# Performance work log

Measured on AMD Instinct MI355X. Metric: run time of the kernel, lower is better.

Reference implementation:

```python
import jax, jax.numpy as jnp
import numpy as np

NF = 16   # channels (nf)
HID = 32  # radial MLP hidden
L = 3     # n_layers
EPS = 1e-8


def fully_connected(N):
    # matches connect_fully(): all (i,j), i != j, row-major over src i
    idx = np.arange(N)
    src, dst = np.meshgrid(idx, idx, indexing='ij')
    mask = src != dst
    return jnp.asarray(src[mask]), jnp.asarray(dst[mask])


def setup_inputs() -> dict:
    key = jax.random.key(0)
    ks = jax.random.split(key, 12)
    B, N, c = 32, 64, NF
    return {
        "pos": jax.random.normal(ks[0], (B * N, 3), jnp.float32),
        "v": jax.random.normal(ks[1], (B * N, 3), jnp.float32),
        "z": jax.random.uniform(ks[2], (B * N,), jnp.float32),
        "w_s_in": jax.random.normal(ks[3], (1, c), jnp.float32) * 0.5,
        "w_v_in": jax.random.normal(ks[4], (1, c), jnp.float32) * 0.5,
        "radial_w1": jax.random.normal(ks[5], (L, 1, HID), jnp.float32) * 0.5,
        "radial_b1": jnp.zeros((L, HID), jnp.float32),
        "radial_w2": jax.random.normal(ks[6], (L, HID, 4 * c * c), jnp.float32) * (1.0 / np.sqrt(HID)),
        "radial_b2": jnp.zeros((L, 4 * c * c), jnp.float32),
        "self_ws": jax.random.normal(ks[7], (L, c, c), jnp.float32) * (1.0 / np.sqrt(c)),
        "self_wv": jax.random.normal(ks[8], (L, c, c), jnp.float32) * (1.0 / np.sqrt(c)),
        "w_v_out": jax.random.normal(ks[9], (c, 1), jnp.float32) * (1.0 / np.sqrt(c)),
        "B": 32,
        "N": 64,
    }


def _tfn_forward(pos, v, z, w_s_in, w_v_in, radial_w1, radial_b1,
                 radial_w2, radial_b2, self_ws, self_wv, w_v_out, B, N):
    c = NF
    src, dst = fully_connected(N)              # [E], E = N*(N-1)
    xs = pos.reshape(B, N, 3)
    vs = v.reshape(B, N, 3)
    # degree-0 (scalar) and degree-1 (vector) node features
    s = z.reshape(B, N, 1) @ w_s_in                                  # [B,N,c]
    vec = vs[:, :, None, :] * w_v_in[0][None, None, :, None]        # [B,N,c,3]
    # per-edge relative geometry (xs[dst] - xs[src], as in source)
    d = xs[:, dst] - xs[:, src]                                      # [B,E,3]
    r = jnp.linalg.norm(d, axis=-1, keepdims=True)                   # [B,E,1]
    u = d / (r + EPS)                                                # unit dir
    for l in range(L):
        # radial network -> per-edge kernel weights (TFN radial kernels)
        h = jax.nn.relu(r @ radial_w1[l] + radial_b1[l])             # [B,E,HID]
        k = h @ radial_w2[l] + radial_b2[l]                          # [B,E,4*c*c]
        W = k.reshape(B, k.shape[1], 4, c, c)
        Wss, Wsv, Wvs, Wvv = W[:, :, 0], W[:, :, 1], W[:, :, 2], W[:, :, 3]
        s_src = s[:, src]                                            # [B,E,c]
        v_src = vec[:, src]                                          # [B,E,c,3]
        v_dot = jnp.einsum('becd,bed->bec', v_src, u)                # 1->0 contraction
        # messages (equivariant): scalar and vector channels
        m_s = jnp.einsum('beij,bej->bei', Wss, s_src) \
            + jnp.einsum('beij,bej->bei', Wvs, v_dot)                # [B,E,c]
        m_v = jnp.einsum('beij,bejd->beid', Wvv, v_src) \
            + jnp.einsum('beij,bej->bei', Wsv, s_src)[..., None] * u[:, :, None, :]  # [B,E,c,3]
        # scatter-aggregate onto destination nodes
        agg_s = jnp.zeros_like(s).at[:, dst].add(m_s)
        agg_v = jnp.zeros_like(vec).at[:, dst].add(m_v)
        # self-interaction + residual (ReLU only on invariant channels)
        s = jax.nn.relu(agg_s @ self_ws[l]) + s
        vec = jnp.einsum('bncd,ce->bned', agg_v, self_wv[l]) + vec
    out_v = jnp.einsum('bncd,c->bnd', vec, w_v_out[:, 0])            # [B,N,3]  (G_out['1'])
    return (out_v + xs).reshape(-1, 3)                               # data.x


def reference(pos, v, z, w_s_in, w_v_in, radial_w1, radial_b1,
              radial_w2, radial_b2, self_ws, self_wv, w_v_out, B, N):
    return _tfn_forward(pos, v, z, w_s_in, w_v_in, radial_w1, radial_b1,
                        radial_w2, radial_b2, self_ws, self_wv, w_v_out, B, N)
```

## Files before the change

kernel.cpp:

```cpp
#include <hip/hip_runtime.h>

#define NF 16
#define NB 32
#define NN 64
#define EPSV 1e-8f

typedef _Float16 f16x8 __attribute__((ext_vector_type(8)));
typedef _Float16 f16x2 __attribute__((ext_vector_type(2)));
typedef __fp16 fp16x2 __attribute__((ext_vector_type(2)));
typedef float f32x4 __attribute__((ext_vector_type(4)));

#define SA_OFF    0
#define VA_OFF    32768
#define SB_OFF    131072
#define VB_OFF    163840
#define AGGSA_OFF 262144
#define AGGVA_OFF 524288
#define AGGSB_OFF 1310720
#define AGGVB_OFF 1572864
#define W2R_OFF   2359296

__device__ __forceinline__ f16x2 cvt_pk(float a, float b) {
    fp16x2 r = __builtin_amdgcn_cvt_pkrtz(a, b);
    return __builtin_bit_cast(f16x2, r);
}

__device__ __forceinline__ f16x8 pack8(f16x2 a, f16x2 b, f16x2 c, f16x2 d) {
    f16x8 r;
    r[0] = a[0]; r[1] = a[1]; r[2] = b[0]; r[3] = b[1];
    r[4] = c[0]; r[5] = c[1]; r[6] = d[0]; r[7] = d[1];
    return r;
}

__device__ __forceinline__ int strm_of(int cc) {
    return (cc == 0) ? 0 : (cc == 1) ? 1 : (cc <= 4) ? 2 : 3;
}

template <int LAYER>
__global__ __launch_bounds__(256, 2) void k_medge(
        const float* __restrict__ pos,
        const float* __restrict__ z, const float* __restrict__ v,
        const float* __restrict__ w_s_in, const float* __restrict__ w_v_in,
        const float* __restrict__ sws_l, const float* __restrict__ swv_l,
        const float* __restrict__ sprev, const float* __restrict__ vprev,
        float* __restrict__ snew, float* __restrict__ vnew,
        const float* __restrict__ aggs_in, const float* __restrict__ aggv_in,
        const float* __restrict__ rw2d, float* __restrict__ W2R,
        const float* __restrict__ b2,
        const float* __restrict__ w1, const float* __restrict__ b1,
        float* __restrict__ aggs_out, float* __restrict__ aggv_out) {
    int blk = blockIdx.x;
    int xcd = blk & 7;
    int t = blk >> 3;
    int b = xcd * 4 + (t >> 4);
    int rem = t & 15;
    int sgrp = rem >> 1, wfh = rem & 1;
    int tid = threadIdx.x;
    int nbase = b * NN + sgrp * 8;

    __shared__ float pos_sh[NN * 3];
    __shared__ float s_sh[8][16];
    __shared__ float vec_t[3][8][16];
    __shared__ float aggfull[8][64];
    __shared__ float sigA_sh[8];
    __shared__ int eexp_sh[8];
    __shared__ _Float16 A2sh[8][2048];
    __shared__ float B2sh[8][64];

    if (tid < NN * 3) pos_sh[tid] = pos[(size_t)b * NN * 3 + tid];

    int fh_p = tid & 63, hq8_p = tid >> 6;
    int fg_p = wfh * 64 + fh_p;
    int i_p = fg_p >> 3, cc_p = fg_p & 7;
    int strm_p = strm_of(cc_p);
    int dd_p = (cc_p <= 1) ? 0 : (cc_p <= 4 ? cc_p - 2 : cc_p - 5);
    float4 wr_all[8][4];
    if (LAYER == 0) {
        const float* wp_p = rw2d + (size_t)(hq8_p * 8) * 1024 + strm_p * 256 + i_p * 16;
#pragma unroll
        for (int h8 = 0; h8 < 8; ++h8) {
            const float4* w4 = (const float4*)(wp_p + h8 * 1024);
            wr_all[h8][0] = w4[0]; wr_all[h8][1] = w4[1];
            wr_all[h8][2] = w4[2]; wr_all[h8][3] = w4[3];
        }
        if (tid < 64) {
            int idxq = 16384 + blk * 64 + tid;
            int fh  = idxq & 63;
            int jq  = (idxq >> 6) & 3;
            int h8  = (idxq >> 8) & 7;
            int hq8 = (idxq >> 11) & 3;
            int wfh2 = (idxq >> 13) & 1;
            int l   = idxq >> 14;
            int fg = wfh2 * 64 + fh;
            int i2 = fg >> 3, cc2 = fg & 7;
            int h = hq8 * 8 + h8;
            ((float4*)W2R)[idxq] = *(const float4*)(rw2d + (size_t)l * 32768 + h * 1024
                                                    + strm_of(cc2) * 256 + i2 * 16 + jq * 4);
        }
    } else {
        const float* wp_p = W2R + (size_t)(((LAYER * 2 + wfh) * 4 + hq8_p) * 8) * 1024
                            + fh_p * 4;
#pragma unroll
        for (int h8 = 0; h8 < 8; ++h8) {
#pragma unroll
            for (int jq = 0; jq < 4; ++jq) {
                wr_all[h8][jq] = *(const float4*)(wp_p + (h8 * 4 + jq) * 256);
            }
        }
    }
    float4 bw_p[4];
    if (hq8_p == 0) {
        const float4* bp = (const float4*)(b2 + strm_p * 256 + i_p * 16);
        bw_p[0] = bp[0]; bw_p[1] = bp[1]; bw_p[2] = bp[2]; bw_p[3] = bp[3];
    }

    if (LAYER == 0) {
        for (int it = tid; it < 512; it += 256) {
            int k = it >> 6, ch = it & 63;
            int node = nbase + k;
            if (ch < 16) {
                float val = z[node] * w_s_in[ch];
                s_sh[k][ch] = val;
                if (wfh == 0) snew[node * 16 + ch] = val;
            } else {
                int q = ch - 16, e = q / 3, d = q % 3;
                float val = v[node * 3 + d] * w_v_in[e];
                vec_t[d][k][e] = val;
                if (wfh == 0) vnew[node * 48 + q] = val;
            }
        }
    } else {
        float resid[2];
        {
            int ii = 0;
            for (int it = tid; it < 512; it += 256, ++ii) {
                int k = it >> 6, ch = it & 63;
                int node = nbase + k;
                float a = 0.f;
                if (ch < 16) {
#pragma unroll
                    for (int p = 0; p < 8; ++p) a += aggs_in[(size_t)p * 32768 + node * 16 + ch];
                    resid[ii] = sprev[node * 16 + ch];
                } else {
#pragma unroll
                    for (int p = 0; p < 8; ++p) a += aggv_in[(size_t)p * 98304 + node * 48 + (ch - 16)];
                    resid[ii] = vprev[node * 48 + (ch - 16)];
                }
                aggfull[k][ch] = a;
            }
        }
        __syncthreads();
        {
            int ii = 0;
            for (int it = tid; it < 512; it += 256, ++ii) {
                int k = it >> 6, ch = it & 63;
                int node = nbase + k;
                if (ch < 16) {
                    float acc = 0.f;
#pragma unroll
                    for (int c = 0; c < 16; ++c) acc += aggfull[k][c] * sws_l[c * 16 + ch];
                    float val = resid[ii] + fmaxf(acc, 0.f);
                    s_sh[k][ch] = val;
                    if (LAYER == 1 && wfh == 0) snew[node * 16 + ch] = val;
                } else {
                    int q = ch - 16, e = q / 3, d = q % 3;
                    float acc = 0.f;
#pragma unroll
                    for (int c = 0; c < 16; ++c) acc += aggfull[k][16 + c * 3 + d] * swv_l[c * 16 + e];
                    float val = resid[ii] + acc;
                    vec_t[d][k][e] = val;
                    if (LAYER == 1 && wfh == 0) vnew[node * 48 + q] = val;
                }
            }
        }
    }
    __syncthreads();

    if (tid < 64) {
        int nk = tid >> 3, sub = tid & 7;
        float m = 0.f;
#pragma unroll
        for (int e = 0; e < 8; ++e) {
            int idx = sub * 8 + e;
            float x = (idx < 16) ? s_sh[nk][idx] : vec_t[(idx - 16) >> 4][nk][(idx - 16) & 15];
            m = fmaxf(m, fabsf(x));
        }
        m = fmaxf(m, __shfl_xor(m, 1));
        m = fmaxf(m, __shfl_xor(m, 2));
        m = fmaxf(m, __shfl_xor(m, 4));
        if (sub == 0) {
            unsigned mb = __float_as_uint(m);
            int ex = (int)((mb >> 23) & 0xFF);
            eexp_sh[nk] = ex - 126;
            sigA_sh[nk] = __uint_as_float((unsigned)(253 - ex) << 23);
        }
    }
    __syncthreads();

    {
        int mt = fh_p >> 4, colw = fh_p & 15;
        int chunk = mt * 64 + hq8_p * 16 + ((colw + hq8_p * 4) & 15);
#pragma unroll
        for (int k2 = 0; k2 < 8; ++k2) {
            const float* srcp = (strm_p <= 1) ? &s_sh[k2][0] : &vec_t[dd_p][k2][0];
            const float4* f4 = (const float4*)srcp;
            float4 f0 = f4[0], f1 = f4[1], f2 = f4[2], f3 = f4[3];
            float sA = sigA_sh[k2];
            f16x8 st;
#pragma unroll
            for (int h8 = 0; h8 < 8; ++h8) {
                float4 a0 = wr_all[h8][0], a1 = wr_all[h8][1];
                float4 a2 = wr_all[h8][2], a3 = wr_all[h8][3];
                float acc = a0.x * f0.x + a0.y * f0.y + a0.z * f0.z + a0.w * f0.w
                          + a1.x * f1.x + a1.y * f1.y + a1.z * f1.z + a1.w * f1.w
                          + a2.x * f2.x + a2.y * f2.y + a2.z * f2.z + a2.w * f2.w
                          + a3.x * f3.x + a3.y * f3.y + a3.z * f3.z + a3.w * f3.w;
                st[h8] = (_Float16)(acc * sA);
            }
            *(f16x8*)&A2sh[k2][chunk * 8] = st;
            if (hq8_p == 0) {
                float accb = bw_p[0].x * f0.x + bw_p[0].y * f0.y + bw_p[0].z * f0.z + bw_p[0].w * f0.w
                           + bw_p[1].x * f1.x + bw_p[1].y * f1.y + bw_p[1].z * f1.z + bw_p[1].w * f1.w
                           + bw_p[2].x * f2.x + bw_p[2].y * f2.y + bw_p[2].z * f2.z + bw_p[2].w * f2.w
                           + bw_p[3].x * f3.x + bw_p[3].y * f3.y + bw_p[3].z * f3.z + bw_p[3].w * f3.w;
                B2sh[k2][fh_p] = accb;
            }
        }
    }
    __syncthreads();

    {
        int wd = tid >> 6;
        int lane = tid & 63;
        int q = lane >> 4, col = lane & 15;
        int dst = wd * 16 + col;
        float qodd = (float)(q & 1);
        float o1 = qodd;

        float pdx = pos_sh[dst * 3 + 0], pdy = pos_sh[dst * 3 + 1], pdz = pos_sh[dst * 3 + 2];
        float w1r[8], b1r[8];
#pragma unroll
        for (int j = 0; j < 8; ++j) { w1r[j] = w1[q * 8 + j]; b1r[j] = b1[q * 8 + j]; }

        int es[8], eblk = -10000;
#pragma unroll
        for (int j = 0; j < 8; ++j) {
            es[j] = eexp_sh[j];
            eblk = es[j] > eblk ? es[j] : eblk;
        }
        float invsb = __uint_as_float((unsigned)(127 + eblk) << 23);

        f32x4 acc[4][4];
#pragma unroll
        for (int mt = 0; mt < 4; ++mt)
#pragma unroll
            for (int u = 0; u < 4; ++u) acc[mt][u] = (f32x4){0.f, 0.f, 0.f, 0.f};
        float ms_p[4] = {0.f, 0.f, 0.f, 0.f};
        float mv_p[4][3];
#pragma unroll
        for (int mt = 0; mt < 4; ++mt) { mv_p[mt][0] = 0.f; mv_p[mt][1] = 0.f; mv_p[mt][2] = 0.f; }

        for (int j = 0; j < 8; ++j) {
            int src = sgrp * 8 + j;
            float psx = pos_sh[src * 3 + 0];
            float psy = pos_sh[src * 3 + 1];
            float psz = pos_sh[src * 3 + 2];
            float dx = pdx - psx, dy = pdy - psy, dz = pdz - psz;
            float r = __builtin_amdgcn_sqrtf(dx * dx + dy * dy + dz * dz);
            float inv = __builtin_amdgcn_rcpf(r + EPSV);
            float ux = dx * inv, uy = dy * inv, uz = dz * inv;
            float vmask = (dst == src) ? 0.f : 1.f;

            int dEx = es[j] - eblk;
            float sc2 = (dEx < -120) ? 0.f : __uint_as_float((unsigned)(127 + dEx) << 23);
            float scl = sc2 * vmask;

            f16x2 ux2 = {(_Float16)ux, (_Float16)ux};
            f16x2 uy2 = {(_Float16)uy, (_Float16)uy};
            f16x2 uz2 = {(_Float16)uz, (_Float16)uz};
            f16x2 p0[4], p1[4], p2[4], p3[4];
#pragma unroll
            for (int jp = 0; jp < 4; ++jp) {
                float h0 = fmaxf(fmaf(r, w1r[2 * jp],     b1r[2 * jp]),     0.f) * scl;
                float h1 = fmaxf(fmaf(r, w1r[2 * jp + 1], b1r[2 * jp + 1]), 0.f) * scl;
                p0[jp] = cvt_pk(h0, h1);
                p1[jp] = p0[jp] * ux2;
                p2[jp] = p0[jp] * uy2;
                p3[jp] = p0[jp] * uz2;
            }
            f16x8 bf0 = pack8(p0[0], p0[1], p0[2], p0[3]);
            f16x8 bf1 = pack8(p1[0], p1[1], p1[2], p1[3]);
            f16x8 bf2 = pack8(p2[0], p2[1], p2[2], p2[3]);
            f16x8 bf3 = pack8(p3[0], p3[1], p3[2], p3[3]);

#pragma unroll
            for (int mt = 0; mt < 4; ++mt) {
                f16x8 af = *(const f16x8*)&A2sh[j][(mt * 64 + q * 16 + ((col + q * 4) & 15)) * 8];
                acc[mt][0] = __builtin_amdgcn_mfma_f32_16x16x32_f16(af, bf0, acc[mt][0], 0, 0, 0);
                acc[mt][1] = __builtin_amdgcn_mfma_f32_16x16x32_f16(af, bf1, acc[mt][1], 0, 0, 0);
                acc[mt][2] = __builtin_amdgcn_mfma_f32_16x16x32_f16(af, bf2, acc[mt][2], 0, 0, 0);
                acc[mt][3] = __builtin_amdgcn_mfma_f32_16x16x32_f16(af, bf3, acc[mt][3], 0, 0, 0);
            }

            float s0  = qodd ? uz : 1.f;
            float zx  = qodd ? 0.f : ux;
            float zy  = qodd ? 0.f : uy;
            float exu = qodd ? 1.f : ux;
            float euy = qodd ? 0.f : uy;
            float euz = qodd ? 0.f : uz;
#pragma unroll
            for (int mt = 0; mt < 4; ++mt) {
                float4 bv = *(const float4*)&B2sh[j][mt * 16 + q * 4];
                float t0 = bv.x * vmask, t1 = bv.y * vmask, t2 = bv.z * vmask, t3 = bv.w * vmask;
                ms_p[mt]    += t0 * s0 + t2 * zx + t3 * zy;
                mv_p[mt][0] += t1 * exu;
                mv_p[mt][1] += t1 * euy + t2 * o1;
                mv_p[mt][2] += t1 * euz + t3 * o1;
            }
        }

#pragma unroll
        for (int mt = 0; mt < 4; ++mt) {
            float fs, fv0, fv1, fv2;
            if ((q & 1) == 0) {
                fs  = acc[mt][0][0] + acc[mt][1][2] + acc[mt][2][3];
                fv0 = acc[mt][1][1]; fv1 = acc[mt][2][1]; fv2 = acc[mt][3][1];
            } else {
                fs  = acc[mt][3][0];
                fv0 = acc[mt][0][1]; fv1 = acc[mt][0][2]; fv2 = acc[mt][0][3];
            }
            ms_p[mt]    += fs  * invsb;
            mv_p[mt][0] += fv0 * invsb;
            mv_p[mt][1] += fv1 * invsb;
            mv_p[mt][2] += fv2 * invsb;
        }

#pragma unroll
        for (int mt = 0; mt < 4; ++mt) {
            ms_p[mt]    += __shfl_xor(ms_p[mt], 16, 64);
            mv_p[mt][0] += __shfl_xor(mv_p[mt][0], 16, 64);
            mv_p[mt][1] += __shfl_xor(mv_p[mt][1], 16, 64);
            mv_p[mt][2] += __shfl_xor(mv_p[mt][2], 16, 64);
        }

        if ((q & 1) == 0) {
            int nodeD = b * NN + dst;
#pragma unroll
            for (int mt = 0; mt < 4; ++mt) {
                int i2 = (wfh * 4 + mt) * 2 + (q >> 1);
                aggs_out[(size_t)sgrp * 32768 + nodeD * 16 + i2] = ms_p[mt];
                float* vp = aggv_out + (size_t)sgrp * 98304 + nodeD * 48 + i2 * 3;
                vp[0] = mv_p[mt][0]; vp[1] = mv_p[mt][1]; vp[2] = mv_p[mt][2];
            }
        }
    }
}

__global__ __launch_bounds__(256) void k_out(
        const float* __restrict__ aggv, const float* __restrict__ wv,
        const float* __restrict__ wvo, const float* __restrict__ vec,
        const float* __restrict__ pos, float* __restrict__ out) {
    int node0 = blockIdx.x * 4;
    int tid = threadIdx.x;
    int k = tid >> 6, t = tid & 63;
    int node = node0 + k;
    __shared__ float avh[4][48];
    __shared__ float vn[4][48];
    if (t < 48) {
        float a = 0.f;
#pragma unroll
        for (int p = 0; p < 8; ++p) a += aggv[(size_t)p * 98304 + node * 48 + t];
        avh[k][t] = a;
    }
    __syncthreads();
    if (t < 48) {
        int e = t / 3, d = t % 3;
        float acc = 0.f;
#pragma unroll
        for (int c = 0; c < 16; ++c) acc += avh[k][c * 3 + d] * wv[c * 16 + e];
        vn[k][t] = (vec[node * 48 + t] + acc) * wvo[e];
    }
    __syncthreads();
    if (t < 3) {
        float acc = 0.f;
#pragma unroll
        for (int e = 0; e < 16; ++e) acc += vn[k][e * 3 + t];
        out[node * 3 + t] = acc + pos[node * 3 + t];
    }
}

extern "C" void kernel_launch(void* const* d_in, const int* in_sizes, int n_in,
                              void* d_out, int out_size, void* d_ws, size_t ws_size,
                              hipStream_t stream) {
    const float* pos = (const float*)d_in[0];
    const float* v   = (const float*)d_in[1];
    const float* z   = (const float*)d_in[2];
    const float* w_s_in = (const float*)d_in[3];
    const float* w_v_in = (const float*)d_in[4];
    const float* rw1 = (const float*)d_in[5];
    const float* rb1 = (const float*)d_in[6];
    const float* rw2 = (const float*)d_in[7];
    const float* rb2 = (const float*)d_in[8];
    const float* sws = (const float*)d_in[9];
    const float* swv = (const float*)d_in[10];
    const float* wvo = (const float*)d_in[11];
    float* out = (float*)d_out;

    float* wsf = (float*)d_ws;
    float* sA = wsf + SA_OFF;
    float* vA = wsf + VA_OFF;
    float* sB = wsf + SB_OFF;
    float* vB = wsf + VB_OFF;
    float* aggsA = wsf + AGGSA_OFF;
    float* aggvA = wsf + AGGVA_OFF;
    float* aggsB = wsf + AGGSB_OFF;
    float* aggvB = wsf + AGGVB_OFF;
    float* W2R = wsf + W2R_OFF;

    k_medge<0><<<512, 256, 0, stream>>>(pos, z, v, w_s_in, w_v_in,
                                        sws, swv, sA, vA, sA, vA,
                                        aggsB, aggvB,
                                        rw2, W2R, rb2, rw1, rb1,
                                        aggsA, aggvA);
    k_medge<1><<<512, 256, 0, stream>>>(pos, z, v, w_s_in, w_v_in,
                                        sws, swv, sA, vA, sB, vB,
                                        aggsA, aggvA,
                                        rw2, W2R, rb2 + 1024, rw1 + 32, rb1 + 32,
                                        aggsB, aggvB);
    k_medge<2><<<512, 256, 0, stream>>>(pos, z, v, w_s_in, w_v_in,
                                        sws + 256, swv + 256, sB, vB, sA, vA,
                                        aggsB, aggvB,
                                        rw2, W2R, rb2 + 2048, rw1 + 64, rb1 + 64,
                                        aggsA, aggvA);
    k_out<<<512, 256, 0, stream>>>(aggvA, swv + 512, wvo, vB, pos, out);
}
```

Before: 62.80 us.

## Fuse final output projection into layer kernels and drop k_out launch

Removes the separate output kernel. Layer 1 writes the residual part of the output (vec·w_v_out + pos) directly. Layer 2 folds self_wv·w_v_out into a 16-vector and atomically adds its projected vector messages into the output instead of writing per-group aggregates. This saves one launch plus the aggregate write/read traffic, at the cost of float atomics, which make the summation order nondeterministic.

```diff
diff --git a/kernel.cpp b/kernel.cpp
--- a/kernel.cpp
+++ b/kernel.cpp
@@ -42,13 +42,15 @@
         const float* __restrict__ z, const float* __restrict__ v,
         const float* __restrict__ w_s_in, const float* __restrict__ w_v_in,
         const float* __restrict__ sws_l, const float* __restrict__ swv_l,
+        const float* __restrict__ swv_out, const float* __restrict__ wvo,
         const float* __restrict__ sprev, const float* __restrict__ vprev,
         float* __restrict__ snew, float* __restrict__ vnew,
         const float* __restrict__ aggs_in, const float* __restrict__ aggv_in,
         const float* __restrict__ rw2d, float* __restrict__ W2R,
         const float* __restrict__ b2,
         const float* __restrict__ w1, const float* __restrict__ b1,
-        float* __restrict__ aggs_out, float* __restrict__ aggv_out) {
+        float* __restrict__ aggs_out, float* __restrict__ aggv_out,
+        float* __restrict__ outp) {
     int blk = blockIdx.x;
     int xcd = blk & 7;
     int t = blk >> 3;
@@ -64,6 +66,7 @@
     __shared__ float aggfull[8][64];
     __shared__ float sigA_sh[8];
     __shared__ int eexp_sh[8];
+    __shared__ float wvo2_sh[16];
     __shared__ _Float16 A2sh[8][2048];
     __shared__ float B2sh[8][64];
 
@@ -176,6 +179,15 @@
     }
     __syncthreads();
 
+    if (LAYER == 1 && wfh == 0 && tid < 24) {
+        int kk = tid / 3, d = tid % 3;
+        float acc = 0.f;
+#pragma unroll
+        for (int e = 0; e < 16; ++e) acc += vec_t[d][kk][e] * wvo[e];
+        int loc = (sgrp * 8 + kk) * 3 + d;
+        outp[(size_t)b * NN * 3 + loc] = acc + pos_sh[loc];
+    }
+
     if (tid < 64) {
         int nk = tid >> 3, sub = tid & 7;
         float m = 0.f;
@@ -194,6 +206,13 @@
             eexp_sh[nk] = ex - 126;
             sigA_sh[nk] = __uint_as_float((unsigned)(253 - ex) << 23);
         }
+    }
+    if (LAYER == 2 && tid >= 64 && tid < 80) {
+        int c = tid - 64;
+        float acc = 0.f;
+#pragma unroll
+        for (int e = 0; e < 16; ++e) acc += swv_out[c * 16 + e] * wvo[e];
+        wvo2_sh[c] = acc;
     }
     __syncthreads();
 
@@ -345,47 +364,29 @@
 
         if ((q & 1) == 0) {
             int nodeD = b * NN + dst;
-#pragma unroll
-            for (int mt = 0; mt < 4; ++mt) {
-                int i2 = (wfh * 4 + mt) * 2 + (q >> 1);
-                aggs_out[(size_t)sgrp * 32768 + nodeD * 16 + i2] = ms_p[mt];
-                float* vp = aggv_out + (size_t)sgrp * 98304 + nodeD * 48 + i2 * 3;
-                vp[0] = mv_p[mt][0]; vp[1] = mv_p[mt][1]; vp[2] = mv_p[mt][2];
-            }
-        }
-    }
-}
-
-__global__ __launch_bounds__(256) void k_out(
-        const float* __restrict__ aggv, const float* __restrict__ wv,
-        const float* __restrict__ wvo, const float* __restrict__ vec,
-        const float* __restrict__ pos, float* __restrict__ out) {
-    int node0 = blockIdx.x * 4;
-    int tid = threadIdx.x;
-    int k = tid >> 6, t = tid & 63;
-    int node = node0 + k;
-    __shared__ float avh[4][48];
-    __shared__ float vn[4][48];
-    if (t < 48) {
-        float a = 0.f;
-#pragma unroll
-        for (int p = 0; p < 8; ++p) a += aggv[(size_t)p * 98304 + node * 48 + t];
-        avh[k][t] = a;
-    }
-    __syncthreads();
-    if (t < 48) {
-        int e = t / 3, d = t % 3;
-        float acc = 0.f;
-#pragma unroll
-        for (int c = 0; c < 16; ++c) acc += avh[k][c * 3 + d] * wv[c * 16 + e];
-        vn[k][t] = (vec[node * 48 + t] + acc) * wvo[e];
-    }
-    __syncthreads();
-    if (t < 3) {
-        float acc = 0.f;
-#pragma unroll
-        for (int e = 0; e < 16; ++e) acc += vn[k][e * 3 + t];
-        out[node * 3 + t] = acc + pos[node * 3 + t];
+            if (LAYER < 2) {
+#pragma unroll
+                for (int mt = 0; mt < 4; ++mt) {
+                    int i2 = (wfh * 4 + mt) * 2 + (q >> 1);
+                    aggs_out[(size_t)sgrp * 32768 + nodeD * 16 + i2] = ms_p[mt];
+                    float* vp = aggv_out + (size_t)sgrp * 98304 + nodeD * 48 + i2 * 3;
+                    vp[0] = mv_p[mt][0]; vp[1] = mv_p[mt][1]; vp[2] = mv_p[mt][2];
+                }
+            } else {
+                float c0 = 0.f, c1 = 0.f, c2 = 0.f;
+#pragma unroll
+                for (int mt = 0; mt < 4; ++mt) {
+                    int i2 = (wfh * 4 + mt) * 2 + (q >> 1);
+                    float w2v = wvo2_sh[i2];
+                    c0 += mv_p[mt][0] * w2v;
+                    c1 += mv_p[mt][1] * w2v;
+                    c2 += mv_p[mt][2] * w2v;
+                }
+                atomicAdd(&outp[(size_t)nodeD * 3 + 0], c0);
+                atomicAdd(&outp[(size_t)nodeD * 3 + 1], c1);
+                atomicAdd(&outp[(size_t)nodeD * 3 + 2], c2);
+            }
+        }
     }
 }
 
@@ -418,19 +419,18 @@
     float* W2R = wsf + W2R_OFF;
 
     k_medge<0><<<512, 256, 0, stream>>>(pos, z, v, w_s_in, w_v_in,
-                                        sws, swv, sA, vA, sA, vA,
+                                        sws, swv, swv, wvo, sA, vA, sA, vA,
                                         aggsB, aggvB,
                                         rw2, W2R, rb2, rw1, rb1,
-                                        aggsA, aggvA);
+                                        aggsA, aggvA, out);
     k_medge<1><<<512, 256, 0, stream>>>(pos, z, v, w_s_in, w_v_in,
-                                        sws, swv, sA, vA, sB, vB,
+                                        sws, swv, swv, wvo, sA, vA, sB, vB,
                                         aggsA, aggvA,
                                         rw2, W2R, rb2 + 1024, rw1 + 32, rb1 + 32,
-                                        aggsB, aggvB);
+                                        aggsB, aggvB, out);
     k_medge<2><<<512, 256, 0, stream>>>(pos, z, v, w_s_in, w_v_in,
-                                        sws + 256, swv + 256, sB, vB, sA, vA,
+                                        sws + 256, swv + 256, swv + 512, wvo, sB, vB, sA, vA,
                                         aggsB, aggvB,
                                         rw2, W2R, rb2 + 2048, rw1 + 64, rb1 + 64,
-                                        aggsA, aggvA);
-    k_out<<<512, 256, 0, stream>>>(aggvA, swv + 512, wvo, vB, pos, out);
+                                        aggsA, aggvA, out);
 }
```

Result: no change. 63.77 us (+1.6%).
